# Kernel optimization log

Hardware: AMD Instinct MI355X
Metric: run time of the kernel (lower is better)

## Reference

```python
import jax, jax.numpy as jnp
import numpy as np

EPS = 1e-4          # var_epsilon for VDP batch norm
DROP = 0.2          # dropout rate
B, HWIN, K, C, HW1, HW2, UNITS = 16, 28, 5, 16, 24, 12, 10


def setup_inputs() -> dict:
    key = jax.random.key(0)
    k0, k1, k2, k3 = jax.random.split(key, 4)
    x = jax.random.normal(k0, (B, HWIN, HWIN, 1), dtype=jnp.float32)
    w_mu_conv = 0.05 * jax.random.normal(k1, (K, K, 1, C), dtype=jnp.float32)
    w_sigma_conv = jnp.full((C,), -6.9, dtype=jnp.float32)   # ini_sigma
    w_mu_fc = 0.05 * jax.random.normal(k2, (C * HW2 * HW2, UNITS), dtype=jnp.float32)
    w_sigma_fc = jnp.full((UNITS,), -6.9, dtype=jnp.float32)
    # keep-mask for dropout (True = kept), keep prob = 1 - DROP
    drop_mask = jax.random.bernoulli(k3, 1.0 - DROP, (B, HW2, HW2, C))
    return {"x": x, "drop_mask": drop_mask, "w_mu_conv": w_mu_conv,
            "w_sigma_conv": w_sigma_conv, "w_mu_fc": w_mu_fc,
            "w_sigma_fc": w_sigma_fc}


def reference(x, drop_mask, w_mu_conv, w_sigma_conv, w_mu_fc, w_sigma_fc):
    b = x.shape[0]
    p1 = HW1 * HW1      # 576
    p2 = HW2 * HW2      # 144

    # ---- VDP_first_Conv: conv mean + Sigma = softplus(w_sigma) * X X^T ----
    mu = jax.lax.conv_general_dilated(
        x, w_mu_conv, (1, 1), 'VALID',
        dimension_numbers=('NHWC', 'HWIO', 'NHWC'))            # [B,24,24,16]
    # patches: in_channels=1 so channel-major vs spatial-major ordering agree
    patches = jax.lax.conv_general_dilated_patches(
        x, (K, K), (1, 1), 'VALID',
        dimension_numbers=('NHWC', 'HWIO', 'NHWC'))            # [B,24,24,25]
    Xm = patches.reshape(b, p1, K * K)                          # [B,576,25]
    XXT = jnp.einsum('bip,bjp->bij', Xm, Xm)                    # [B,576,576]
    sigma = XXT[..., None] * jax.nn.softplus(w_sigma_conv)      # [B,576,576,16]

    # ---- VDPBatch_Normalization ----
    mean = mu.mean(axis=(0, 1, 2))
    var = mu.var(axis=(0, 1, 2))
    mu = (mu - mean) / jnp.sqrt(var + EPS)
    sigma = sigma / (var + EPS)

    # ---- VDPELU: Sigma *= g g^T with g = d elu / d mu ----
    g = jnp.where(mu > 0, 1.0, jnp.exp(mu))                     # elu'(x)
    mu = jax.nn.elu(mu)
    gf = g.reshape(b, p1, C)
    sigma = sigma * gf[:, :, None, :] * gf[:, None, :, :]

    # ---- VDP_MaxPooling 2x2/2 (24 divisible by 2 -> SAME == no pad) ----
    w = mu.reshape(b, HW2, 2, HW2, 2, C).transpose(0, 1, 3, 2, 4, 5)
    w = w.reshape(b, HW2, HW2, 4, C)                            # window flat (dy,dx)
    arg = jnp.argmax(w, axis=3)                                 # [B,12,12,16]
    mu = jnp.max(w, axis=3)                                     # [B,12,12,16]
    ii = jnp.arange(HW2)
    yy = 2 * ii[None, :, None, None] + arg // 2
    xx = 2 * ii[None, None, :, None] + arg % 2
    idx = yy * HW1 + xx                                         # flat index into 576
    idx_c = idx.transpose(0, 3, 1, 2).reshape(b, C, p2)         # [B,16,144]
    Sc = sigma.transpose(0, 3, 1, 2)                            # [B,16,576,576]
    Sc = jnp.take_along_axis(Sc, idx_c[:, :, :, None], axis=2)  # gather rows
    Sc = jnp.take_along_axis(Sc, idx_c[:, :, None, :], axis=3)  # gather cols -> [B,16,144,144]

    # ---- VDPDropout (training) ----
    scale = 1.0 / (1.0 - DROP)
    keep = drop_mask.astype(mu.dtype)                           # [B,12,12,16]
    mu = mu * keep * scale
    m = keep.transpose(0, 3, 1, 2).reshape(b, C, p2)
    Sc = (scale ** 2) * Sc * m[:, :, :, None] * m[:, :, None, :]

    # ---- VDP_Flatten_and_FC ----
    mu_flat = mu.reshape(b, -1)                                 # NHWC flatten
    mu_out = mu_flat @ w_mu_fc                                  # [B,10]
    W1 = w_mu_fc.reshape(C, p2, UNITS)                          # as in original code
    S1 = jnp.einsum('ciu,bcij,cjv->buv', W1, Sc, W1)            # sum_c W^T Sigma W
    sp = jax.nn.softplus(w_sigma_fc)                            # [10]
    tr = jnp.trace(Sc, axis1=2, axis2=3).sum(axis=1)            # [B]
    diag = sp[None, :] * (tr[:, None] + jnp.sum(mu_flat * mu_flat, axis=1)[:, None])
    Sigma_out = S1 + diag[:, :, None] * jnp.eye(UNITS, dtype=S1.dtype)
    return mu_out, Sigma_out
```

## Files before the change

### kernel.cpp

```cpp
#include <hip/hip_runtime.h>
#include <math.h>

#define EPSV   1e-4f
#define DSCALE 1.25f

#define XSTR 30
#define XIMG 840
#define QPAD 148
#define FLAG_MAGIC 0x1F2E3D4C


__device__ __forceinline__ float wave_sum(float v) {
#pragma unroll
    for (int off = 32; off > 0; off >>= 1) v += __shfl_down(v, off, 64);
    return v;
}

__global__ __launch_bounds__(256) void kFused(
    const float* __restrict__ x,
    const int*   __restrict__ dmask,
    const float* __restrict__ wconv,
    const float* __restrict__ wsconv,
    const float* __restrict__ wfc,
    const float* __restrict__ wsfc,
    float* __restrict__ moP, float* __restrict__ s1P, float* __restrict__ tmP,
    int*   __restrict__ flags,
    float* __restrict__ out)
{
    __shared__ __align__(16) float xa_s[16 * XIMG];
    __shared__ __align__(16) float W1_s[1440];
    __shared__ __align__(8)  float W2_s[1440];
    __shared__ __align__(16) float fWT_s[10 * QPAD];
    __shared__ __align__(16) float XgT_s[25 * QPAD];
    __shared__ float w_s[25];
    __shared__ float mu_s[576];
    __shared__ float red_s[8];
    __shared__ float f_s[144], mud_s[144];
    __shared__ int   I_s[144];
    __shared__ float T_s[250];
    __shared__ float stat_s[8];
    __shared__ float spfc_s[10];
    __shared__ float tmg_s[16];

    const int bc = blockIdx.x, b = bc & 15, c = bc >> 4, t = threadIdx.x;
    const bool is_red = (c == 0);

    const int dm = (t < 144) ? dmask[b * 2304 + t * 16 + c] : 0;
    const float wsc_v = wsconv[c];

    {
        const float4* x4 = (const float4*)x;
        for (int j4 = t; j4 < 3136; j4 += 256) {
            const int bb  = j4 / 196;
            const int rem = j4 - bb * 196;
            const int r   = rem / 7;
            const int c4  = (rem - r * 7) * 4;
            const float4 v = x4[j4];
            float* dst = &xa_s[bb * XIMG + r * XSTR + c4];
            ((float2*)dst)[0] = make_float2(v.x, v.y);
            ((float2*)dst)[1] = make_float2(v.z, v.w);
        }
    }
    {
        const float4* wfc4 = (const float4*)wfc;
        for (int j4 = t; j4 < 360; j4 += 256)
            ((float4*)W1_s)[j4] = wfc4[c * 360 + j4];
    }
    {
        const float2* wfc2 = (const float2*)wfc;
        for (int j2 = t; j2 < 720; j2 += 256) {
            const int q = j2 / 5, uh = j2 - q * 5;
            ((float2*)W2_s)[j2] = wfc2[(q * 16 + c) * 5 + uh];
        }
    }
    if (t < 25) w_s[t] = wconv[t * 16 + c];
    if (t < 10) spfc_s[t] = log1pf(expf(wsfc[t]));
    __syncthreads();

    float s_acc = 0.f, q_acc = 0.f;
    for (int task = t; task < 768; task += 256) {
        const int bb = task / 48;
        const int hr = task - bb * 48;
        const int row = hr >> 1;
        const int x0 = (hr & 1) * 12;
        const float* xb = &xa_s[bb * XIMG + row * XSTR + x0];
        float acc[12];
#pragma unroll
        for (int j = 0; j < 12; j++) acc[j] = 0.f;
#pragma unroll
        for (int dy = 0; dy < 5; dy++) {
            const float2* xr2 = (const float2*)(xb + dy * XSTR);
            float rr[16];
#pragma unroll
            for (int k = 0; k < 8; k++) {
                const float2 v = xr2[k];
                rr[2 * k] = v.x; rr[2 * k + 1] = v.y;
            }
#pragma unroll
            for (int dx = 0; dx < 5; dx++) {
                const float wv = w_s[dy * 5 + dx];
#pragma unroll
                for (int j = 0; j < 12; j++)
                    acc[j] = fmaf(rr[j + dx], wv, acc[j]);
            }
        }
        const int obase = row * 24 + x0;
        if (bb == b) {
#pragma unroll
            for (int j = 0; j < 12; j++) mu_s[obase + j] = acc[j];
        }
#pragma unroll
        for (int j = 0; j < 12; j++) {
            s_acc += acc[j];
            q_acc = fmaf(acc[j], acc[j], q_acc);
        }
    }
    {
        const float ws1 = wave_sum(s_acc), ws2 = wave_sum(q_acc);
        if ((t & 63) == 0) { red_s[t >> 6] = ws1; red_s[4 + (t >> 6)] = ws2; }
    }
    __syncthreads();
    if (t == 0) {
        const float ts = red_s[0] + red_s[1] + red_s[2] + red_s[3];
        const float tq = red_s[4] + red_s[5] + red_s[6] + red_s[7];
        const float mean = ts * (1.f / 9216.f);
        const float var  = tq * (1.f / 9216.f) - mean * mean;
        stat_s[0] = mean;
        stat_s[1] = 1.f / sqrtf(var + EPSV);
        stat_s[2] = log1pf(expf(wsc_v)) / (var + EPSV);
    }
    __syncthreads();

    float trv = 0.f, mmv = 0.f;
    if (t < 144) {
        const int h = t / 12, w2 = t - h * 12;
        const int y0 = 2 * h, x0 = 2 * w2;
        const int i0 = y0 * 24 + x0;
        const float v00 = mu_s[i0], v01 = mu_s[i0 + 1];
        const float v10 = mu_s[i0 + 24], v11 = mu_s[i0 + 25];
        float best = v00; int arg = 0;
        if (v01 > best) { best = v01; arg = 1; }
        if (v10 > best) { best = v10; arg = 2; }
        if (v11 > best) { best = v11; arg = 3; }
        const int yy = y0 + (arg >> 1), xx = x0 + (arg & 1);
        const int ipos = yy * XSTR + xx;
        const float vn = (best - stat_s[0]) * stat_s[1];
        const float m = (dm != 0) ? 1.f : 0.f;
        const float g  = vn > 0.f ? 1.f : expf(vn);
        const float el = vn > 0.f ? vn  : expm1f(vn);
        const float fq = DSCALE * m * g;
        const float md = DSCALE * m * el;
        f_s[t] = fq; mud_s[t] = md; I_s[t] = ipos;
        const float* xo = &xa_s[b * XIMG + ipos];
        float pn = 0.f;
#pragma unroll
        for (int dy = 0; dy < 5; dy++)
#pragma unroll
            for (int dx = 0; dx < 5; dx++) {
                const float v = xo[dy * XSTR + dx];
                pn = fmaf(v, v, pn);
            }
        trv = stat_s[2] * fq * fq * pn;
        mmv = md * md;
    }
    {
        const float wt = wave_sum(trv), wm = wave_sum(mmv);
        if ((t & 63) == 0) { red_s[t >> 6] = wt; red_s[4 + (t >> 6)] = wm; }
    }
    __syncthreads();

    for (int j = t; j < 1440; j += 256) {
        const int q = j / 10, u = j - q * 10;
        fWT_s[u * QPAD + q] = f_s[q] * W1_s[j];
    }
    {
        const int bo = b * XIMG;
        for (int e = t; e < 3600; e += 256) {
            const int p = e / 144, q = e - p * 144;
            XgT_s[p * QPAD + q] = xa_s[bo + I_s[q] + (p / 5) * XSTR + (p % 5)];
        }
    }
    if (t == 0)
        stat_s[3] = red_s[0] + red_s[1] + red_s[2] + red_s[3]
                  + red_s[4] + red_s[5] + red_s[6] + red_s[7];
    __syncthreads();

    if (t < 250) {
        const int p = t / 10, u = t - (t / 10) * 10;
        const float4* fa = (const float4*)&fWT_s[u * QPAD];
        const float4* xg = (const float4*)&XgT_s[p * QPAD];
        float acc = 0.f;
#pragma unroll 6
        for (int k = 0; k < 36; k++) {
            const float4 a = fa[k], g4 = xg[k];
            acc = fmaf(a.x, g4.x, acc);
            acc = fmaf(a.y, g4.y, acc);
            acc = fmaf(a.z, g4.z, acc);
            acc = fmaf(a.w, g4.w, acc);
        }
        T_s[t] = acc;
    }
    __syncthreads();

    float sig_val = 0.f, mu_val = 0.f;
    if (t < 100) {
        const int u = t / 10, v = t - (t / 10) * 10;
        float acc = 0.f;
#pragma unroll
        for (int p = 0; p < 25; p++)
            acc = fmaf(T_s[p * 10 + u], T_s[p * 10 + v], acc);
        sig_val = stat_s[2] * acc;
    } else if (t < 110) {
        const int u = t - 100;
        float acc = 0.f;
#pragma unroll 8
        for (int q = 0; q < 144; q++)
            acc = fmaf(mud_s[q], W2_s[q * 10 + u], acc);
        mu_val = acc;
    }

    if (!is_red) {
        if (t < 100)
            __hip_atomic_store(&s1P[bc * 100 + t], sig_val,
                               __ATOMIC_RELAXED, __HIP_MEMORY_SCOPE_AGENT);
        else if (t < 110)
            __hip_atomic_store(&moP[bc * 10 + (t - 100)], mu_val,
                               __ATOMIC_RELAXED, __HIP_MEMORY_SCOPE_AGENT);
        else if (t == 110)
            __hip_atomic_store(&tmP[bc], stat_s[3],
                               __ATOMIC_RELAXED, __HIP_MEMORY_SCOPE_AGENT);
        asm volatile("s_waitcnt vmcnt(0)" ::: "memory");
        __syncthreads();
        if (t == 0)
            __hip_atomic_store(&flags[bc * 32], FLAG_MAGIC,
                               __ATOMIC_RELAXED, __HIP_MEMORY_SCOPE_AGENT);
    } else {
        if (t < 15) {
            const int idx = ((t + 1) * 16 + b) * 32;
            while (__hip_atomic_load(&flags[idx], __ATOMIC_RELAXED,
                                     __HIP_MEMORY_SCOPE_AGENT) != FLAG_MAGIC)
                __builtin_amdgcn_s_sleep(2);
            __hip_atomic_store(&flags[idx], 0,
                               __ATOMIC_RELAXED, __HIP_MEMORY_SCOPE_AGENT);
        }
        __syncthreads();
        if (t < 15)
            tmg_s[t] = __hip_atomic_load(&tmP[(t + 1) * 16 + b],
                                         __ATOMIC_RELAXED, __HIP_MEMORY_SCOPE_AGENT);
        __syncthreads();
        if (t == 0) {
            float a = stat_s[3];
            for (int i = 0; i < 15; i++) a += tmg_s[i];
            stat_s[5] = a;
        }
        __syncthreads();
        if (t < 100) {
            const int u = t / 10, v = t - (t / 10) * 10;
            float acc = sig_val;
#pragma unroll
            for (int cc = 1; cc < 16; cc++)
                acc += __hip_atomic_load(&s1P[(cc * 16 + b) * 100 + t],
                                         __ATOMIC_RELAXED, __HIP_MEMORY_SCOPE_AGENT);
            if (u == v) acc += spfc_s[u] * stat_s[5];
            out[160 + b * 100 + t] = acc;
        } else if (t < 110) {
            const int u = t - 100;
            float acc = mu_val;
#pragma unroll
            for (int cc = 1; cc < 16; cc++)
                acc += __hip_atomic_load(&moP[(cc * 16 + b) * 10 + u],
                                         __ATOMIC_RELAXED, __HIP_MEMORY_SCOPE_AGENT);
            out[b * 10 + u] = acc;
        }
    }
}

extern "C" void kernel_launch(void* const* d_in, const int* in_sizes, int n_in,
                              void* d_out, int out_size, void* d_ws, size_t ws_size,
                              hipStream_t stream) {
    const float* x      = (const float*)d_in[0];
    const int*   dmask  = (const int*)d_in[1];
    const float* wconv  = (const float*)d_in[2];
    const float* wsconv = (const float*)d_in[3];
    const float* wfc    = (const float*)d_in[4];
    const float* wsfc   = (const float*)d_in[5];
    float* out = (float*)d_out;

    float* ws    = (float*)d_ws;
    float* moP   = ws;
    float* s1P   = ws + 2560;
    float* tmP   = ws + 28160;
    int*   flags = (int*)(ws + 28416);

    kFused<<<256, 256, 0, stream>>>(x, dmask, wconv, wsconv, wfc, wsfc,
                                    moP, s1P, tmP, flags, out);
}
```

Before: 21.25 us.

## Compute batch-norm stats via cross-block flag exchange instead of redundant full-batch conv

Previously every block loaded all 16 images and recomputed the whole conv to get per-channel batch statistics. Now each block convolves only its own image, computing the 2x2 pool window directly per thread with patch norms fused in. Per-block partial sums go to global memory, a designated block per channel (b==0) reduces them and publishes mean/istd/scale through flags. This cuts redundant conv work and shared memory use, but adds two grid-wide spin-wait handoffs that rely on all 256 blocks being co-resident.

```diff
diff --git a/kernel.cpp b/kernel.cpp
--- a/kernel.cpp
+++ b/kernel.cpp
@@ -15,6 +15,9 @@
     for (int off = 32; off > 0; off >>= 1) v += __shfl_down(v, off, 64);
     return v;
 }
+
+#define AG_LD(p)    __hip_atomic_load((p), __ATOMIC_RELAXED, __HIP_MEMORY_SCOPE_AGENT)
+#define AG_ST(p, v) __hip_atomic_store((p), (v), __ATOMIC_RELAXED, __HIP_MEMORY_SCOPE_AGENT)
 
 __global__ __launch_bounds__(256) void kFused(
     const float* __restrict__ x,
@@ -24,16 +27,16 @@
     const float* __restrict__ wfc,
     const float* __restrict__ wsfc,
     float* __restrict__ moP, float* __restrict__ s1P, float* __restrict__ tmP,
-    int*   __restrict__ flags,
+    int* __restrict__ flagB, int* __restrict__ flagA, float* __restrict__ dataA,
+    int* __restrict__ flagS, float* __restrict__ dataS,
     float* __restrict__ out)
 {
-    __shared__ __align__(16) float xa_s[16 * XIMG];
+    __shared__ __align__(16) float xa_s[XIMG];
     __shared__ __align__(16) float W1_s[1440];
     __shared__ __align__(8)  float W2_s[1440];
     __shared__ __align__(16) float fWT_s[10 * QPAD];
     __shared__ __align__(16) float XgT_s[25 * QPAD];
     __shared__ float w_s[25];
-    __shared__ float mu_s[576];
     __shared__ float red_s[8];
     __shared__ float f_s[144], mud_s[144];
     __shared__ int   I_s[144];
@@ -43,20 +46,16 @@
     __shared__ float tmg_s[16];
 
     const int bc = blockIdx.x, b = bc & 15, c = bc >> 4, t = threadIdx.x;
-    const bool is_red = (c == 0);
-
-    const int dm = (t < 144) ? dmask[b * 2304 + t * 16 + c] : 0;
+
+    const int   dm    = (t < 144) ? dmask[b * 2304 + t * 16 + c] : 0;
     const float wsc_v = wsconv[c];
 
     {
-        const float4* x4 = (const float4*)x;
-        for (int j4 = t; j4 < 3136; j4 += 256) {
-            const int bb  = j4 / 196;
-            const int rem = j4 - bb * 196;
-            const int r   = rem / 7;
-            const int c4  = (rem - r * 7) * 4;
-            const float4 v = x4[j4];
-            float* dst = &xa_s[bb * XIMG + r * XSTR + c4];
+        const float4* x4 = (const float4*)(x + b * 784);
+        if (t < 196) {
+            const int r = t / 7, c4 = (t - r * 7) * 4;
+            const float4 v = x4[t];
+            float* dst = &xa_s[r * XSTR + c4];
             ((float2*)dst)[0] = make_float2(v.x, v.y);
             ((float2*)dst)[1] = make_float2(v.z, v.w);
         }
@@ -77,89 +76,110 @@
     if (t < 10) spfc_s[t] = log1pf(expf(wsfc[t]));
     __syncthreads();
 
-    float s_acc = 0.f, q_acc = 0.f;
-    for (int task = t; task < 768; task += 256) {
-        const int bb = task / 48;
-        const int hr = task - bb * 48;
-        const int row = hr >> 1;
-        const int x0 = (hr & 1) * 12;
-        const float* xb = &xa_s[bb * XIMG + row * XSTR + x0];
-        float acc[12];
-#pragma unroll
-        for (int j = 0; j < 12; j++) acc[j] = 0.f;
-#pragma unroll
-        for (int dy = 0; dy < 5; dy++) {
-            const float2* xr2 = (const float2*)(xb + dy * XSTR);
-            float rr[16];
-#pragma unroll
-            for (int k = 0; k < 8; k++) {
-                const float2 v = xr2[k];
-                rr[2 * k] = v.x; rr[2 * k + 1] = v.y;
+    float best = 0.f, pn = 0.f;
+    float psum_part = 0.f, psq_part = 0.f;
+    if (t < 144) {
+        const int h = t / 12, w2 = t - h * 12;
+        const int y0 = 2 * h, x0 = 2 * w2;
+        float xr[6][6];
+#pragma unroll
+        for (int i = 0; i < 6; i++) {
+            const float2* row = (const float2*)&xa_s[(y0 + i) * XSTR + x0];
+#pragma unroll
+            for (int k = 0; k < 3; k++) {
+                const float2 v = row[k];
+                xr[i][2 * k] = v.x; xr[i][2 * k + 1] = v.y;
             }
-#pragma unroll
-            for (int dx = 0; dx < 5; dx++) {
-                const float wv = w_s[dy * 5 + dx];
-#pragma unroll
-                for (int j = 0; j < 12; j++)
-                    acc[j] = fmaf(rr[j + dx], wv, acc[j]);
+        }
+        float v00 = 0.f, v01 = 0.f, v10 = 0.f, v11 = 0.f;
+#pragma unroll
+        for (int i = 0; i < 5; i++)
+#pragma unroll
+            for (int j = 0; j < 5; j++) {
+                const float wv = w_s[i * 5 + j];
+                v00 = fmaf(xr[i][j],         wv, v00);
+                v01 = fmaf(xr[i][j + 1],     wv, v01);
+                v10 = fmaf(xr[i + 1][j],     wv, v10);
+                v11 = fmaf(xr[i + 1][j + 1], wv, v11);
             }
-        }
-        const int obase = row * 24 + x0;
-        if (bb == b) {
-#pragma unroll
-            for (int j = 0; j < 12; j++) mu_s[obase + j] = acc[j];
-        }
-#pragma unroll
-        for (int j = 0; j < 12; j++) {
-            s_acc += acc[j];
-            q_acc = fmaf(acc[j], acc[j], q_acc);
-        }
-    }
-    {
-        const float ws1 = wave_sum(s_acc), ws2 = wave_sum(q_acc);
-        if ((t & 63) == 0) { red_s[t >> 6] = ws1; red_s[4 + (t >> 6)] = ws2; }
-    }
-    __syncthreads();
+        psum_part = v00 + v01 + v10 + v11;
+        psq_part  = v00 * v00 + v01 * v01 + v10 * v10 + v11 * v11;
+        best = v00; int arg = 0;
+        if (v01 > best) { best = v01; arg = 1; }
+        if (v10 > best) { best = v10; arg = 2; }
+        if (v11 > best) { best = v11; arg = 3; }
+        float pn0 = 0.f, pn1 = 0.f, pn2 = 0.f, pn3 = 0.f;
+#pragma unroll
+        for (int i = 0; i < 5; i++)
+#pragma unroll
+            for (int j = 0; j < 5; j++) {
+                pn0 = fmaf(xr[i][j],         xr[i][j],         pn0);
+                pn1 = fmaf(xr[i][j + 1],     xr[i][j + 1],     pn1);
+                pn2 = fmaf(xr[i + 1][j],     xr[i + 1][j],     pn2);
+                pn3 = fmaf(xr[i + 1][j + 1], xr[i + 1][j + 1], pn3);
+            }
+        pn = (arg == 0) ? pn0 : (arg == 1) ? pn1 : (arg == 2) ? pn2 : pn3;
+        I_s[t] = (y0 + (arg >> 1)) * XSTR + (x0 + (arg & 1));
+    }
+    {
+        const float wsum1 = wave_sum(psum_part), wsum2 = wave_sum(psq_part);
+        if ((t & 63) == 0) { red_s[t >> 6] = wsum1; red_s[4 + (t >> 6)] = wsum2; }
+    }
+    __syncthreads();
+
     if (t == 0) {
         const float ts = red_s[0] + red_s[1] + red_s[2] + red_s[3];
         const float tq = red_s[4] + red_s[5] + red_s[6] + red_s[7];
-        const float mean = ts * (1.f / 9216.f);
-        const float var  = tq * (1.f / 9216.f) - mean * mean;
-        stat_s[0] = mean;
-        stat_s[1] = 1.f / sqrtf(var + EPSV);
-        stat_s[2] = log1pf(expf(wsc_v)) / (var + EPSV);
+        const int ln = bc * 32;
+        AG_ST(&dataA[ln], ts); AG_ST(&dataA[ln + 1], tq);
+        asm volatile("s_waitcnt vmcnt(0)" ::: "memory");
+        AG_ST(&flagA[ln], FLAG_MAGIC);
+    }
+
+    if (b == 0 && t < 16) {
+        const int ln = (c * 16 + t) * 32;
+        while (AG_LD(&flagA[ln]) != FLAG_MAGIC) __builtin_amdgcn_s_sleep(1);
+        AG_ST(&flagA[ln], 0);
+        float pa = AG_LD(&dataA[ln]), pb = AG_LD(&dataA[ln + 1]);
+#pragma unroll
+        for (int off = 8; off > 0; off >>= 1) {
+            pa += __shfl_down(pa, off, 64);
+            pb += __shfl_down(pb, off, 64);
+        }
+        pa = __shfl(pa, 0, 64); pb = __shfl(pb, 0, 64);
+        const float mean = pa * (1.f / 9216.f);
+        const float var  = pb * (1.f / 9216.f) - mean * mean;
+        const float istd = 1.f / sqrtf(var + EPSV);
+        const float scv  = log1pf(expf(wsc_v)) / (var + EPSV);
+        AG_ST(&dataS[ln], mean); AG_ST(&dataS[ln + 1], istd); AG_ST(&dataS[ln + 2], scv);
+        asm volatile("s_waitcnt vmcnt(0)" ::: "memory");
+        AG_ST(&flagS[ln], FLAG_MAGIC);
+    }
+
+    for (int e = t; e < 3600; e += 256) {
+        const int p = e / 144, q = e - p * 144;
+        XgT_s[p * QPAD + q] = xa_s[I_s[q] + (p / 5) * XSTR + (p % 5)];
+    }
+
+    if (t == 0) {
+        const int ln = bc * 32;
+        while (AG_LD(&flagS[ln]) != FLAG_MAGIC) __builtin_amdgcn_s_sleep(1);
+        AG_ST(&flagS[ln], 0);
+        stat_s[0] = AG_LD(&dataS[ln]);
+        stat_s[1] = AG_LD(&dataS[ln + 1]);
+        stat_s[2] = AG_LD(&dataS[ln + 2]);
     }
     __syncthreads();
 
     float trv = 0.f, mmv = 0.f;
     if (t < 144) {
-        const int h = t / 12, w2 = t - h * 12;
-        const int y0 = 2 * h, x0 = 2 * w2;
-        const int i0 = y0 * 24 + x0;
-        const float v00 = mu_s[i0], v01 = mu_s[i0 + 1];
-        const float v10 = mu_s[i0 + 24], v11 = mu_s[i0 + 25];
-        float best = v00; int arg = 0;
-        if (v01 > best) { best = v01; arg = 1; }
-        if (v10 > best) { best = v10; arg = 2; }
-        if (v11 > best) { best = v11; arg = 3; }
-        const int yy = y0 + (arg >> 1), xx = x0 + (arg & 1);
-        const int ipos = yy * XSTR + xx;
         const float vn = (best - stat_s[0]) * stat_s[1];
-        const float m = (dm != 0) ? 1.f : 0.f;
+        const float m  = (dm != 0) ? 1.f : 0.f;
         const float g  = vn > 0.f ? 1.f : expf(vn);
         const float el = vn > 0.f ? vn  : expm1f(vn);
         const float fq = DSCALE * m * g;
         const float md = DSCALE * m * el;
-        f_s[t] = fq; mud_s[t] = md; I_s[t] = ipos;
-        const float* xo = &xa_s[b * XIMG + ipos];
-        float pn = 0.f;
-#pragma unroll
-        for (int dy = 0; dy < 5; dy++)
-#pragma unroll
-            for (int dx = 0; dx < 5; dx++) {
-                const float v = xo[dy * XSTR + dx];
-                pn = fmaf(v, v, pn);
-            }
+        f_s[t] = fq; mud_s[t] = md;
         trv = stat_s[2] * fq * fq * pn;
         mmv = md * md;
     }
@@ -172,13 +192,6 @@
     for (int j = t; j < 1440; j += 256) {
         const int q = j / 10, u = j - q * 10;
         fWT_s[u * QPAD + q] = f_s[q] * W1_s[j];
-    }
-    {
-        const int bo = b * XIMG;
-        for (int e = t; e < 3600; e += 256) {
-            const int p = e / 144, q = e - p * 144;
-            XgT_s[p * QPAD + q] = xa_s[bo + I_s[q] + (p / 5) * XSTR + (p % 5)];
-        }
     }
     if (t == 0)
         stat_s[3] = red_s[0] + red_s[1] + red_s[2] + red_s[3]
@@ -219,34 +232,21 @@
         mu_val = acc;
     }
 
-    if (!is_red) {
-        if (t < 100)
-            __hip_atomic_store(&s1P[bc * 100 + t], sig_val,
-                               __ATOMIC_RELAXED, __HIP_MEMORY_SCOPE_AGENT);
-        else if (t < 110)
-            __hip_atomic_store(&moP[bc * 10 + (t - 100)], mu_val,
-                               __ATOMIC_RELAXED, __HIP_MEMORY_SCOPE_AGENT);
-        else if (t == 110)
-            __hip_atomic_store(&tmP[bc], stat_s[3],
-                               __ATOMIC_RELAXED, __HIP_MEMORY_SCOPE_AGENT);
+    if (c != 0) {
+        if (t < 100)       AG_ST(&s1P[bc * 100 + t], sig_val);
+        else if (t < 110)  AG_ST(&moP[bc * 10 + (t - 100)], mu_val);
+        else if (t == 110) AG_ST(&tmP[bc], stat_s[3]);
         asm volatile("s_waitcnt vmcnt(0)" ::: "memory");
         __syncthreads();
-        if (t == 0)
-            __hip_atomic_store(&flags[bc * 32], FLAG_MAGIC,
-                               __ATOMIC_RELAXED, __HIP_MEMORY_SCOPE_AGENT);
+        if (t == 0) AG_ST(&flagB[bc * 32], FLAG_MAGIC);
     } else {
         if (t < 15) {
             const int idx = ((t + 1) * 16 + b) * 32;
-            while (__hip_atomic_load(&flags[idx], __ATOMIC_RELAXED,
-                                     __HIP_MEMORY_SCOPE_AGENT) != FLAG_MAGIC)
-                __builtin_amdgcn_s_sleep(2);
-            __hip_atomic_store(&flags[idx], 0,
-                               __ATOMIC_RELAXED, __HIP_MEMORY_SCOPE_AGENT);
+            while (AG_LD(&flagB[idx]) != FLAG_MAGIC) __builtin_amdgcn_s_sleep(2);
+            AG_ST(&flagB[idx], 0);
         }
         __syncthreads();
-        if (t < 15)
-            tmg_s[t] = __hip_atomic_load(&tmP[(t + 1) * 16 + b],
-                                         __ATOMIC_RELAXED, __HIP_MEMORY_SCOPE_AGENT);
+        if (t < 15) tmg_s[t] = AG_LD(&tmP[(t + 1) * 16 + b]);
         __syncthreads();
         if (t == 0) {
             float a = stat_s[3];
@@ -259,8 +259,7 @@
             float acc = sig_val;
 #pragma unroll
             for (int cc = 1; cc < 16; cc++)
-                acc += __hip_atomic_load(&s1P[(cc * 16 + b) * 100 + t],
-                                         __ATOMIC_RELAXED, __HIP_MEMORY_SCOPE_AGENT);
+                acc += AG_LD(&s1P[(cc * 16 + b) * 100 + t]);
             if (u == v) acc += spfc_s[u] * stat_s[5];
             out[160 + b * 100 + t] = acc;
         } else if (t < 110) {
@@ -268,8 +267,7 @@
             float acc = mu_val;
 #pragma unroll
             for (int cc = 1; cc < 16; cc++)
-                acc += __hip_atomic_load(&moP[(cc * 16 + b) * 10 + u],
-                                         __ATOMIC_RELAXED, __HIP_MEMORY_SCOPE_AGENT);
+                acc += AG_LD(&moP[(cc * 16 + b) * 10 + u]);
             out[b * 10 + u] = acc;
         }
     }
@@ -290,8 +288,13 @@
     float* moP   = ws;
     float* s1P   = ws + 2560;
     float* tmP   = ws + 28160;
-    int*   flags = (int*)(ws + 28416);
+    int*   flagB = (int*)(ws + 28416);
+    int*   flagA = (int*)(ws + 36608);
+    float* dataA = ws + 44800;
+    int*   flagS = (int*)(ws + 52992);
+    float* dataS = ws + 61184;
 
     kFused<<<256, 256, 0, stream>>>(x, dmask, wconv, wsconv, wfc, wsfc,
-                                    moP, s1P, tmP, flags, out);
+                                    moP, s1P, tmP, flagB, flagA, dataA,
+                                    flagS, dataS, out);
 }
```

Measured after the change: 18.34 us. 1.16x faster.
